# Optimization experiments

Hardware: AMD Instinct MI355X
Metric: run time of the kernel (lower is better)

## Reference

```python
import jax, jax.numpy as jnp
import numpy as np

N = 65536
E = 1048576
NFEAT, NHID, NCLASS = 128, 64, 40


def setup_inputs() -> dict:
    key = jax.random.key(0)
    ks = jax.random.split(key, 20)
    inp = {
        "x": jax.random.normal(ks[0], (N, NFEAT), dtype=jnp.float32),
        "src": jax.random.randint(ks[1], (E,), 0, N, dtype=jnp.int32),
        "dst": jax.random.randint(ks[2], (E,), 0, N, dtype=jnp.int32),
        "edge_w": jax.random.uniform(ks[3], (E,), dtype=jnp.float32),
    }
    dims = [(NFEAT, NHID)] + [(NHID, NHID)] * 5 + [(NHID, NCLASS)]
    for i, (fi, fo) in enumerate(dims, start=1):
        scale = 1.0 / np.sqrt(fi)
        inp[f"W{i}"] = jax.random.uniform(ks[3 + i], (fi, fo), minval=-scale, maxval=scale, dtype=jnp.float32)
        inp[f"b{i}"] = jax.random.uniform(ks[10 + i], (fo,), minval=-scale, maxval=scale, dtype=jnp.float32)
    return inp


def _gc(h, W, b, src, dst, edge_w):
    # GraphConvolution: adj @ (h @ W) + b, with adj in COO form.
    support = h @ W                      # [N, fo] dense GEMM
    msgs = support[src] * edge_w[:, None]  # [E, fo] irregular gather
    agg = jax.ops.segment_sum(msgs, dst, num_segments=N)  # scatter-add
    return agg + b


def reference(x, src, dst, edge_w, W1, b1, W2, b2, W3, b3, W4, b4, W5, b5, W6, b6, W7, b7):
    # eval mode: dropout is identity
    h = jax.nn.relu(_gc(x, W1, b1, src, dst, edge_w))
    h = jax.nn.relu(_gc(h, W2, b2, src, dst, edge_w))
    h = jax.nn.relu(_gc(h, W3, b3, src, dst, edge_w)) + h
    h = jax.nn.relu(_gc(h, W4, b4, src, dst, edge_w)) + h
    h = jax.nn.relu(_gc(h, W5, b5, src, dst, edge_w)) + h
    h = jax.nn.relu(_gc(h, W6, b6, src, dst, edge_w))
    h = _gc(h, W7, b7, src, dst, edge_w)
    return jax.nn.log_softmax(h, axis=1)
```

## Files before the change

### kernel.cpp

```cpp
#include <hip/hip_runtime.h>
#include <math.h>


constexpr int NFEAT = 128, NHID = 64, NCLASS = 40;

typedef unsigned short ushort_t;
typedef int ivec4 __attribute__((ext_vector_type(4)));

__device__ inline float bf2f(ushort_t u) {
  union { unsigned int i; float f; } v; v.i = ((unsigned int)u) << 16; return v.f;
}
__device__ inline ushort_t f2bf(float f) {
  union { float f; unsigned int i; } v; v.f = f;
  unsigned int lsb = (v.i >> 16) & 1u;
  v.i += 0x7fffu + lsb;
  return (ushort_t)(v.i >> 16);
}

__global__ void rank_k(const int* __restrict__ dst, int* __restrict__ cnt4,
                       int* __restrict__ rank, int E, int N) {
  int i = blockIdx.x * blockDim.x + threadIdx.x;
  int base = i * 4;
  if (base >= E) return;
  int4 d4 = *(const int4*)(dst + base);
  int r0 = atomicAdd(&cnt4[0 * N + d4.x], 1);
  int r1 = atomicAdd(&cnt4[1 * N + d4.y], 1);
  int r2 = atomicAdd(&cnt4[2 * N + d4.z], 1);
  int r3 = atomicAdd(&cnt4[3 * N + d4.w], 1);
  ivec4 rr = { (r0 << 2) | 0, (r1 << 2) | 1, (r2 << 2) | 2, (r3 << 2) | 3 };
  __builtin_nontemporal_store(rr, (ivec4*)(rank + base));
}

__global__ void scan1_k(const int* __restrict__ cnt4, int* __restrict__ off,
                        int* __restrict__ bsum, int4* __restrict__ sb4, int n) {
  __shared__ int tmp[256];
  int tid = threadIdx.x;
  int i = blockIdx.x * 256 + tid;
  int c0 = 0, c1 = 0, c2 = 0, c3 = 0;
  if (i < n) {
    c0 = cnt4[i]; c1 = cnt4[n + i]; c2 = cnt4[2 * n + i]; c3 = cnt4[3 * n + i];
  }
  int v = c0 + c1 + c2 + c3;
  tmp[tid] = v;
  __syncthreads();
  for (int d = 1; d < 256; d <<= 1) {
    int t = (tid >= d) ? tmp[tid - d] : 0;
    __syncthreads();
    tmp[tid] += t;
    __syncthreads();
  }
  if (i < n) {
    off[i] = tmp[tid] - v;
    sb4[i] = make_int4(0, c0, c0 + c1, c0 + c1 + c2);
  }
  if (tid == 255) bsum[blockIdx.x] = tmp[255];
}

__global__ void scan2_k(int* __restrict__ bsum, int nb) {
  __shared__ int tmp[256];
  int tid = threadIdx.x;
  int v = (tid < nb) ? bsum[tid] : 0;
  tmp[tid] = v;
  __syncthreads();
  for (int d = 1; d < 256; d <<= 1) {
    int t = (tid >= d) ? tmp[tid - d] : 0;
    __syncthreads();
    tmp[tid] += t;
    __syncthreads();
  }
  if (tid < nb) bsum[tid] = tmp[tid] - v;
}

__global__ void scan3_k(int* __restrict__ off, const int* __restrict__ bsum, int n, int E) {
  int i = blockIdx.x * blockDim.x + threadIdx.x;
  if (i < n) off[i] += bsum[i >> 8];
  if (i == 0) off[n] = E;
}

__global__ void fill_k(const int* __restrict__ src, const int* __restrict__ dst,
                       const float* __restrict__ w, const int* __restrict__ off,
                       const int* __restrict__ rank, const int* __restrict__ sb4,
                       int2* __restrict__ edata, int E) {
  int i = blockIdx.x * blockDim.x + threadIdx.x;
  if (i < E) {
    int d = dst[i];
    int rp = rank[i];
    int s = rp & 3, sr = rp >> 2;
    int pos = off[d] + sb4[d * 4 + s] + sr;
    int2 v = make_int2(src[i], __float_as_int(w[i]));
    __builtin_nontemporal_store(*(const long long*)&v, (long long*)&edata[pos]);
  }
}

template<int FI, int FO>
__global__ __launch_bounds__(256) void gemm_k(const float* __restrict__ h,
                                              const float* __restrict__ W,
                                              ushort_t* __restrict__ out, int n) {
  constexpr int HS = 68;
  __shared__ float hl[64 * HS];
  __shared__ float wl[64 * 64];
  int tid = threadIdx.x;
  int row0 = blockIdx.x * 64;
  int tx = tid & 15, ty = tid >> 4;

  float acc[4][4] = {};

  for (int kc = 0; kc < FI; kc += 64) {
    {
      const float* hb = h + (size_t)row0 * FI + kc;
      for (int i = tid; i < 64 * 16; i += 256) {
        int r = i >> 4, kk = (i & 15) << 2;
        float4 v = *(const float4*)(hb + (size_t)r * FI + kk);
        *(float4*)&hl[r * HS + kk] = v;
      }
    }
    if (FO == 64) {
      const float4* Wb = (const float4*)(W + (size_t)kc * 64);
      for (int i = tid; i < 64 * 16; i += 256) ((float4*)wl)[i] = Wb[i];
    } else {
      for (int i = tid; i < 64 * 64; i += 256) wl[i] = 0.0f;
      __syncthreads();
      for (int i = tid; i < 64 * FO; i += 256)
        wl[(i / FO) * 64 + (i % FO)] = W[(size_t)(kc + i / FO) * FO + (i % FO)];
    }
    __syncthreads();

    for (int k4 = 0; k4 < 64; k4 += 4) {
      float4 a[4];
#pragma unroll
      for (int r = 0; r < 4; ++r)
        a[r] = *(const float4*)&hl[(ty * 4 + r) * HS + k4];
#pragma unroll
      for (int j = 0; j < 4; ++j) {
        float4 bv = *(const float4*)&wl[(k4 + j) * 64 + tx * 4];
        const float* bp = (const float*)&bv;
#pragma unroll
        for (int r = 0; r < 4; ++r) {
          const float* ap = (const float*)&a[r];
#pragma unroll
          for (int c = 0; c < 4; ++c) acc[r][c] += ap[j] * bp[c];
        }
      }
    }
    __syncthreads();
  }

  if (FO == 64) {
#pragma unroll
    for (int r = 0; r < 4; ++r) {
      ushort_t pk[4];
#pragma unroll
      for (int c = 0; c < 4; ++c) pk[c] = f2bf(acc[r][c]);
      *(ushort4*)&out[(size_t)(row0 + ty * 4 + r) * 64 + tx * 4] =
          make_ushort4(pk[0], pk[1], pk[2], pk[3]);
    }
  } else {
#pragma unroll
    for (int r = 0; r < 4; ++r)
#pragma unroll
      for (int c = 0; c < 4; ++c) {
        int col = tx * 4 + c;
        if (col < FO) out[(size_t)(row0 + ty * 4 + r) * FO + col] = f2bf(acc[r][c]);
      }
  }
}

__global__ __launch_bounds__(256, 8) void agg_k(
    const ushort_t* __restrict__ support,
    const int2* __restrict__ edata,
    const int* __restrict__ off,
    const float* __restrict__ bias,
    const float* __restrict__ resid,
    float* __restrict__ out,
    int n, int do_relu) {
  int tid = blockIdx.x * blockDim.x + threadIdx.x;
  int wid = tid >> 6, lane = tid & 63;
  if (wid >= n) return;
  int half = lane >> 5;
  int hl   = lane & 31;
  int e0 = __builtin_amdgcn_readfirstlane(off[wid]);
  int e1 = __builtin_amdgcn_readfirstlane(off[wid + 1]);
  int deg = e1 - e0;

  const ushort_t* sp = support + hl * 2;
  const int* epi = (const int*)(edata + e0);

  float ax[4] = {}, ay[4] = {};
  if (deg > 0) {
    int sx[16];
#pragma unroll
    for (int j = 0; j < 16; ++j) {
      int rel = 2 * j + half;
      sx[j] = epi[(rel < deg ? rel : 0) * 2];
    }
    unsigned int u[16];
#pragma unroll
    for (int j = 0; j < 16; ++j)
      u[j] = *(const unsigned int*)(sp + ((size_t)sx[j] << 6));
    float wv[16];
#pragma unroll
    for (int j = 0; j < 16; ++j) {
      int rel = 2 * j + half;
      wv[j] = (rel < deg) ? __int_as_float(epi[rel * 2 + 1]) : 0.0f;
    }
#pragma unroll
    for (int j = 0; j < 16; ++j) {
      ax[j & 3] += wv[j] * __int_as_float(u[j] << 16);
      ay[j & 3] += wv[j] * __int_as_float(u[j] & 0xffff0000u);
    }
    for (int it = 32; it < deg; it += 16) {
      int2 ed[8];
#pragma unroll
      for (int j = 0; j < 8; ++j) {
        int rel = it + 2 * j + half;
        ed[j] = *(const int2*)(epi + (rel < deg ? rel : 0) * 2);
      }
      unsigned int uu[8];
#pragma unroll
      for (int j = 0; j < 8; ++j)
        uu[j] = *(const unsigned int*)(sp + ((size_t)ed[j].x << 6));
#pragma unroll
      for (int j = 0; j < 8; ++j) {
        int rel = it + 2 * j + half;
        float w = (rel < deg) ? __int_as_float(ed[j].y) : 0.0f;
        ax[j & 3] += w * __int_as_float(uu[j] << 16);
        ay[j & 3] += w * __int_as_float(uu[j] & 0xffff0000u);
      }
    }
  }
  float sx2 = (ax[0] + ax[1]) + (ax[2] + ax[3]);
  float sy2 = (ay[0] + ay[1]) + (ay[2] + ay[3]);
  sx2 += __shfl_xor(sx2, 32, 64);
  sy2 += __shfl_xor(sy2, 32, 64);
  if (half == 0) {
    float2 bv = *(const float2*)&bias[hl * 2];
    float vx = sx2 + bv.x, vy = sy2 + bv.y;
    if (do_relu) { vx = fmaxf(vx, 0.0f); vy = fmaxf(vy, 0.0f); }
    if (resid) {
      float2 r = *(const float2*)&resid[(size_t)wid * 64 + hl * 2];
      vx += r.x; vy += r.y;
    }
    *(float2*)&out[(size_t)wid * 64 + hl * 2] = make_float2(vx, vy);
  }
}

__global__ __launch_bounds__(256, 8) void agg_final_k(
    const ushort_t* __restrict__ support,
    const int2* __restrict__ edata,
    const int* __restrict__ off,
    const float* __restrict__ bias,
    float* __restrict__ out, int n) {
  int tid = blockIdx.x * blockDim.x + threadIdx.x;
  int wid = tid >> 6, lane = tid & 63;
  if (wid >= n) return;
  int half = lane >> 5;
  int hl   = lane & 31;
  int col  = (hl < 20 ? hl : 0) * 2;
  int e0 = __builtin_amdgcn_readfirstlane(off[wid]);
  int e1 = __builtin_amdgcn_readfirstlane(off[wid + 1]);
  int deg = e1 - e0;

  const ushort_t* sp = support + col;
  const int* epi = (const int*)(edata + e0);

  float ax[4] = {}, ay[4] = {};
  if (deg > 0) {
    int sx[16];
#pragma unroll
    for (int j = 0; j < 16; ++j) {
      int rel = 2 * j + half;
      sx[j] = epi[(rel < deg ? rel : 0) * 2];
    }
    unsigned int u[16];
#pragma unroll
    for (int j = 0; j < 16; ++j)
      u[j] = *(const unsigned int*)(sp + (size_t)sx[j] * NCLASS);
    float wv[16];
#pragma unroll
    for (int j = 0; j < 16; ++j) {
      int rel = 2 * j + half;
      wv[j] = (rel < deg) ? __int_as_float(epi[rel * 2 + 1]) : 0.0f;
    }
#pragma unroll
    for (int j = 0; j < 16; ++j) {
      ax[j & 3] += wv[j] * __int_as_float(u[j] << 16);
      ay[j & 3] += wv[j] * __int_as_float(u[j] & 0xffff0000u);
    }
    for (int it = 32; it < deg; it += 16) {
      int2 ed[8];
#pragma unroll
      for (int j = 0; j < 8; ++j) {
        int rel = it + 2 * j + half;
        ed[j] = *(const int2*)(epi + (rel < deg ? rel : 0) * 2);
      }
      unsigned int uu[8];
#pragma unroll
      for (int j = 0; j < 8; ++j)
        uu[j] = *(const unsigned int*)(sp + (size_t)ed[j].x * NCLASS);
#pragma unroll
      for (int j = 0; j < 8; ++j) {
        int rel = it + 2 * j + half;
        float w = (rel < deg) ? __int_as_float(ed[j].y) : 0.0f;
        ax[j & 3] += w * __int_as_float(uu[j] << 16);
        ay[j & 3] += w * __int_as_float(uu[j] & 0xffff0000u);
      }
    }
  }
  float sx2 = (ax[0] + ax[1]) + (ax[2] + ax[3]);
  float sy2 = (ay[0] + ay[1]) + (ay[2] + ay[3]);
  sx2 += __shfl_xor(sx2, 32, 64);
  sy2 += __shfl_xor(sy2, 32, 64);
  float2 bv = *(const float2*)&bias[col];
  float vx = sx2 + bv.x, vy = sy2 + bv.y;

  bool valid = (hl < 20);
  float m = valid ? fmaxf(vx, vy) : -INFINITY;
#pragma unroll
  for (int d = 32; d; d >>= 1) m = fmaxf(m, __shfl_xor(m, d, 64));
  float ex = valid ? (expf(vx - m) + expf(vy - m)) : 0.0f;
  float s = ex;
#pragma unroll
  for (int d = 32; d; d >>= 1) s += __shfl_xor(s, d, 64);
  float ls = logf(s);
  if (half == 0 && valid)
    *(float2*)&out[(size_t)wid * NCLASS + hl * 2] = make_float2(vx - m - ls, vy - m - ls);
}

extern "C" void kernel_launch(void* const* d_in, const int* in_sizes, int n_in,
                              void* d_out, int out_size, void* d_ws, size_t ws_size,
                              hipStream_t stream) {
  const float* x   = (const float*)d_in[0];
  const int*   src = (const int*)d_in[1];
  const int*   dst = (const int*)d_in[2];
  const float* ew  = (const float*)d_in[3];
  const float* W[7]; const float* b[7];
  for (int i = 0; i < 7; ++i) {
    W[i] = (const float*)d_in[4 + 2 * i];
    b[i] = (const float*)d_in[5 + 2 * i];
  }
  int N = in_sizes[0] / NFEAT;
  int E = in_sizes[1];

  char* ws = (char*)d_ws;
  int*      off     = (int*)(ws + 0);
  int*      bsum    = (int*)(ws + (1ll << 20));
  int*      cnt4    = (int*)(ws + (2ll << 20));
  int4*     sb4     = (int4*)(ws + (3ll << 20));
  int2*     edata   = (int2*)(ws + (4ll << 20));
  int*      rank    = (int*)(ws + (12ll << 20));
  ushort_t* support = (ushort_t*)(ws + (16ll << 20));
  float*    hA      = (float*)(ws + (32ll << 20));
  float*    hB      = (float*)(ws + (48ll << 20));

  (void)hipMemsetAsync(cnt4, 0, (size_t)4 * N * sizeof(int), stream);
  rank_k<<<(E / 4 + 255) / 256, 256, 0, stream>>>(dst, cnt4, rank, E, N);
  int nb = (N + 255) / 256;
  scan1_k<<<nb, 256, 0, stream>>>(cnt4, off, bsum, sb4, N);
  scan2_k<<<1, 256, 0, stream>>>(bsum, nb);
  scan3_k<<<nb, 256, 0, stream>>>(off, bsum, N, E);
  fill_k<<<(E + 255) / 256, 256, 0, stream>>>(src, dst, ew, off, rank,
                                              (const int*)sb4, edata, E);

  int gb_gemm = N / 64;
  int gb_agg  = N / 4;

  gemm_k<128, 64><<<gb_gemm, 256, 0, stream>>>(x, W[0], support, N);
  agg_k<<<gb_agg, 256, 0, stream>>>(support, edata, off, b[0], nullptr, hA, N, 1);
  gemm_k<64, 64><<<gb_gemm, 256, 0, stream>>>(hA, W[1], support, N);
  agg_k<<<gb_agg, 256, 0, stream>>>(support, edata, off, b[1], nullptr, hB, N, 1);
  gemm_k<64, 64><<<gb_gemm, 256, 0, stream>>>(hB, W[2], support, N);
  agg_k<<<gb_agg, 256, 0, stream>>>(support, edata, off, b[2], hB, hA, N, 1);
  gemm_k<64, 64><<<gb_gemm, 256, 0, stream>>>(hA, W[3], support, N);
  agg_k<<<gb_agg, 256, 0, stream>>>(support, edata, off, b[3], hA, hB, N, 1);
  gemm_k<64, 64><<<gb_gemm, 256, 0, stream>>>(hB, W[4], support, N);
  agg_k<<<gb_agg, 256, 0, stream>>>(support, edata, off, b[4], hB, hA, N, 1);
  gemm_k<64, 64><<<gb_gemm, 256, 0, stream>>>(hA, W[5], support, N);
  agg_k<<<gb_agg, 256, 0, stream>>>(support, edata, off, b[5], nullptr, hB, N, 1);
  gemm_k<64, 40><<<gb_gemm, 256, 0, stream>>>(hB, W[6], support, N);
  agg_final_k<<<gb_agg, 256, 0, stream>>>(support, edata, off, b[6], (float*)d_out, N);
}
```

Baseline: 411.7 us.

## Process two nodes per wavefront in aggregation and vectorize CSR fill kernel

The aggregation kernels now assign two destination nodes to each wavefront, so gathers for both nodes are issued together and more loads are in flight per wave. Occupancy hint drops from 8 to 4 blocks per CU to allow the larger register footprint, and the grid is halved to match. The fill kernel now handles four edges per thread using vector loads of src, dst, weight and rank. Risks are higher register pressure and lower occupancy, plus load imbalance when the two paired nodes have very different degrees.

```diff
diff --git a/kernel.cpp b/kernel.cpp
--- a/kernel.cpp
+++ b/kernel.cpp
@@ -82,12 +82,25 @@
                        const int* __restrict__ rank, const int* __restrict__ sb4,
                        int2* __restrict__ edata, int E) {
   int i = blockIdx.x * blockDim.x + threadIdx.x;
-  if (i < E) {
-    int d = dst[i];
-    int rp = rank[i];
-    int s = rp & 3, sr = rp >> 2;
-    int pos = off[d] + sb4[d * 4 + s] + sr;
-    int2 v = make_int2(src[i], __float_as_int(w[i]));
+  int base = i * 4;
+  if (base >= E) return;
+  int4 s4 = *(const int4*)(src + base);
+  int4 d4 = *(const int4*)(dst + base);
+  float4 w4 = *(const float4*)(w + base);
+  int4 r4 = *(const int4*)(rank + base);
+  int dd[4] = { d4.x, d4.y, d4.z, d4.w };
+  int rr[4] = { r4.x, r4.y, r4.z, r4.w };
+  int ss[4] = { s4.x, s4.y, s4.z, s4.w };
+  float ww[4] = { w4.x, w4.y, w4.z, w4.w };
+  int ob[4], sb[4];
+#pragma unroll
+  for (int k = 0; k < 4; ++k) ob[k] = off[dd[k]];
+#pragma unroll
+  for (int k = 0; k < 4; ++k) sb[k] = sb4[dd[k] * 4 + (rr[k] & 3)];
+#pragma unroll
+  for (int k = 0; k < 4; ++k) {
+    int pos = ob[k] + sb[k] + (rr[k] >> 2);
+    int2 v = make_int2(ss[k], __float_as_int(ww[k]));
     __builtin_nontemporal_store(*(const long long*)&v, (long long*)&edata[pos]);
   }
 }
@@ -165,7 +178,7 @@
   }
 }
 
-__global__ __launch_bounds__(256, 8) void agg_k(
+__global__ __launch_bounds__(256, 4) void agg_k(
     const ushort_t* __restrict__ support,
     const int2* __restrict__ edata,
     const int* __restrict__ off,
@@ -174,156 +187,257 @@
     float* __restrict__ out,
     int n, int do_relu) {
   int tid = blockIdx.x * blockDim.x + threadIdx.x;
-  int wid = tid >> 6, lane = tid & 63;
-  if (wid >= n) return;
+  int p = tid >> 6, lane = tid & 63;
+  int nA = 2 * p, nB = 2 * p + 1;
+  if (nA >= n) return;
   int half = lane >> 5;
   int hl   = lane & 31;
-  int e0 = __builtin_amdgcn_readfirstlane(off[wid]);
-  int e1 = __builtin_amdgcn_readfirstlane(off[wid + 1]);
-  int deg = e1 - e0;
+  int e0a = __builtin_amdgcn_readfirstlane(off[nA]);
+  int e0b = __builtin_amdgcn_readfirstlane(off[nB]);
+  int e1b = __builtin_amdgcn_readfirstlane(off[nB + 1]);
+  int degA = e0b - e0a, degB = e1b - e0b;
 
   const ushort_t* sp = support + hl * 2;
-  const int* epi = (const int*)(edata + e0);
-
-  float ax[4] = {}, ay[4] = {};
-  if (deg > 0) {
-    int sx[16];
-#pragma unroll
-    for (int j = 0; j < 16; ++j) {
-      int rel = 2 * j + half;
-      sx[j] = epi[(rel < deg ? rel : 0) * 2];
-    }
-    unsigned int u[16];
-#pragma unroll
-    for (int j = 0; j < 16; ++j)
-      u[j] = *(const unsigned int*)(sp + ((size_t)sx[j] << 6));
-    float wv[16];
-#pragma unroll
-    for (int j = 0; j < 16; ++j) {
-      int rel = 2 * j + half;
-      wv[j] = (rel < deg) ? __int_as_float(epi[rel * 2 + 1]) : 0.0f;
-    }
-#pragma unroll
-    for (int j = 0; j < 16; ++j) {
-      ax[j & 3] += wv[j] * __int_as_float(u[j] << 16);
-      ay[j & 3] += wv[j] * __int_as_float(u[j] & 0xffff0000u);
-    }
-    for (int it = 32; it < deg; it += 16) {
-      int2 ed[8];
-#pragma unroll
-      for (int j = 0; j < 8; ++j) {
-        int rel = it + 2 * j + half;
-        ed[j] = *(const int2*)(epi + (rel < deg ? rel : 0) * 2);
-      }
-      unsigned int uu[8];
-#pragma unroll
-      for (int j = 0; j < 8; ++j)
-        uu[j] = *(const unsigned int*)(sp + ((size_t)ed[j].x << 6));
-#pragma unroll
-      for (int j = 0; j < 8; ++j) {
-        int rel = it + 2 * j + half;
-        float w = (rel < deg) ? __int_as_float(ed[j].y) : 0.0f;
-        ax[j & 3] += w * __int_as_float(uu[j] << 16);
-        ay[j & 3] += w * __int_as_float(uu[j] & 0xffff0000u);
-      }
-    }
-  }
-  float sx2 = (ax[0] + ax[1]) + (ax[2] + ax[3]);
-  float sy2 = (ay[0] + ay[1]) + (ay[2] + ay[3]);
-  sx2 += __shfl_xor(sx2, 32, 64);
-  sy2 += __shfl_xor(sy2, 32, 64);
+  const int* epA = (const int*)(edata + e0a);
+  const int* epB = (const int*)(edata + e0b);
+
+  float axA[4] = {}, ayA[4] = {}, axB[4] = {}, ayB[4] = {};
+
+  int sA[16], sB[16];
+#pragma unroll
+  for (int j = 0; j < 16; ++j) {
+    int rel = 2 * j + half;
+    sA[j] = epA[(rel < degA ? rel : 0) * 2];
+  }
+#pragma unroll
+  for (int j = 0; j < 16; ++j) {
+    int rel = 2 * j + half;
+    sB[j] = epB[(rel < degB ? rel : 0) * 2];
+  }
+  unsigned int uA[16], uB[16];
+#pragma unroll
+  for (int j = 0; j < 16; ++j)
+    uA[j] = *(const unsigned int*)(sp + ((size_t)sA[j] << 6));
+#pragma unroll
+  for (int j = 0; j < 16; ++j)
+    uB[j] = *(const unsigned int*)(sp + ((size_t)sB[j] << 6));
+#pragma unroll
+  for (int j = 0; j < 16; ++j) {
+    int rel = 2 * j + half;
+    float w = (rel < degA) ? __int_as_float(epA[rel * 2 + 1]) : 0.0f;
+    axA[j & 3] += w * __int_as_float(uA[j] << 16);
+    ayA[j & 3] += w * __int_as_float(uA[j] & 0xffff0000u);
+  }
+#pragma unroll
+  for (int j = 0; j < 16; ++j) {
+    int rel = 2 * j + half;
+    float w = (rel < degB) ? __int_as_float(epB[rel * 2 + 1]) : 0.0f;
+    axB[j & 3] += w * __int_as_float(uB[j] << 16);
+    ayB[j & 3] += w * __int_as_float(uB[j] & 0xffff0000u);
+  }
+  for (int it = 32; it < degA; it += 16) {
+    int2 ed[8];
+#pragma unroll
+    for (int j = 0; j < 8; ++j) {
+      int rel = it + 2 * j + half;
+      ed[j] = *(const int2*)(epA + (rel < degA ? rel : 0) * 2);
+    }
+    unsigned int uu[8];
+#pragma unroll
+    for (int j = 0; j < 8; ++j)
+      uu[j] = *(const unsigned int*)(sp + ((size_t)ed[j].x << 6));
+#pragma unroll
+    for (int j = 0; j < 8; ++j) {
+      int rel = it + 2 * j + half;
+      float w = (rel < degA) ? __int_as_float(ed[j].y) : 0.0f;
+      axA[j & 3] += w * __int_as_float(uu[j] << 16);
+      ayA[j & 3] += w * __int_as_float(uu[j] & 0xffff0000u);
+    }
+  }
+  for (int it = 32; it < degB; it += 16) {
+    int2 ed[8];
+#pragma unroll
+    for (int j = 0; j < 8; ++j) {
+      int rel = it + 2 * j + half;
+      ed[j] = *(const int2*)(epB + (rel < degB ? rel : 0) * 2);
+    }
+    unsigned int uu[8];
+#pragma unroll
+    for (int j = 0; j < 8; ++j)
+      uu[j] = *(const unsigned int*)(sp + ((size_t)ed[j].x << 6));
+#pragma unroll
+    for (int j = 0; j < 8; ++j) {
+      int rel = it + 2 * j + half;
+      float w = (rel < degB) ? __int_as_float(ed[j].y) : 0.0f;
+      axB[j & 3] += w * __int_as_float(uu[j] << 16);
+      ayB[j & 3] += w * __int_as_float(uu[j] & 0xffff0000u);
+    }
+  }
+
+  float sxA = ((axA[0] + axA[1]) + (axA[2] + axA[3]));
+  float syA = ((ayA[0] + ayA[1]) + (ayA[2] + ayA[3]));
+  float sxB = ((axB[0] + axB[1]) + (axB[2] + axB[3]));
+  float syB = ((ayB[0] + ayB[1]) + (ayB[2] + ayB[3]));
+  sxA += __shfl_xor(sxA, 32, 64);
+  syA += __shfl_xor(syA, 32, 64);
+  sxB += __shfl_xor(sxB, 32, 64);
+  syB += __shfl_xor(syB, 32, 64);
+
+  float2 bv = *(const float2*)&bias[hl * 2];
   if (half == 0) {
-    float2 bv = *(const float2*)&bias[hl * 2];
-    float vx = sx2 + bv.x, vy = sy2 + bv.y;
+    float vx = sxA + bv.x, vy = syA + bv.y;
     if (do_relu) { vx = fmaxf(vx, 0.0f); vy = fmaxf(vy, 0.0f); }
     if (resid) {
-      float2 r = *(const float2*)&resid[(size_t)wid * 64 + hl * 2];
+      float2 r = *(const float2*)&resid[(size_t)nA * 64 + hl * 2];
       vx += r.x; vy += r.y;
     }
-    *(float2*)&out[(size_t)wid * 64 + hl * 2] = make_float2(vx, vy);
-  }
-}
-
-__global__ __launch_bounds__(256, 8) void agg_final_k(
+    *(float2*)&out[(size_t)nA * 64 + hl * 2] = make_float2(vx, vy);
+  } else {
+    float vx = sxB + bv.x, vy = syB + bv.y;
+    if (do_relu) { vx = fmaxf(vx, 0.0f); vy = fmaxf(vy, 0.0f); }
+    if (resid) {
+      float2 r = *(const float2*)&resid[(size_t)nB * 64 + hl * 2];
+      vx += r.x; vy += r.y;
+    }
+    *(float2*)&out[(size_t)nB * 64 + hl * 2] = make_float2(vx, vy);
+  }
+}
+
+__global__ __launch_bounds__(256, 4) void agg_final_k(
     const ushort_t* __restrict__ support,
     const int2* __restrict__ edata,
     const int* __restrict__ off,
     const float* __restrict__ bias,
     float* __restrict__ out, int n) {
   int tid = blockIdx.x * blockDim.x + threadIdx.x;
-  int wid = tid >> 6, lane = tid & 63;
-  if (wid >= n) return;
+  int p = tid >> 6, lane = tid & 63;
+  int nA = 2 * p, nB = 2 * p + 1;
+  if (nA >= n) return;
   int half = lane >> 5;
   int hl   = lane & 31;
   int col  = (hl < 20 ? hl : 0) * 2;
-  int e0 = __builtin_amdgcn_readfirstlane(off[wid]);
-  int e1 = __builtin_amdgcn_readfirstlane(off[wid + 1]);
-  int deg = e1 - e0;
+  int e0a = __builtin_amdgcn_readfirstlane(off[nA]);
+  int e0b = __builtin_amdgcn_readfirstlane(off[nB]);
+  int e1b = __builtin_amdgcn_readfirstlane(off[nB + 1]);
+  int degA = e0b - e0a, degB = e1b - e0b;
 
   const ushort_t* sp = support + col;
-  const int* epi = (const int*)(edata + e0);
-
-  float ax[4] = {}, ay[4] = {};
-  if (deg > 0) {
-    int sx[16];
-#pragma unroll
-    for (int j = 0; j < 16; ++j) {
-      int rel = 2 * j + half;
-      sx[j] = epi[(rel < deg ? rel : 0) * 2];
-    }
-    unsigned int u[16];
-#pragma unroll
-    for (int j = 0; j < 16; ++j)
-      u[j] = *(const unsigned int*)(sp + (size_t)sx[j] * NCLASS);
-    float wv[16];
-#pragma unroll
-    for (int j = 0; j < 16; ++j) {
-      int rel = 2 * j + half;
-      wv[j] = (rel < deg) ? __int_as_float(epi[rel * 2 + 1]) : 0.0f;
-    }
-#pragma unroll
-    for (int j = 0; j < 16; ++j) {
-      ax[j & 3] += wv[j] * __int_as_float(u[j] << 16);
-      ay[j & 3] += wv[j] * __int_as_float(u[j] & 0xffff0000u);
-    }
-    for (int it = 32; it < deg; it += 16) {
-      int2 ed[8];
-#pragma unroll
-      for (int j = 0; j < 8; ++j) {
-        int rel = it + 2 * j + half;
-        ed[j] = *(const int2*)(epi + (rel < deg ? rel : 0) * 2);
-      }
-      unsigned int uu[8];
-#pragma unroll
-      for (int j = 0; j < 8; ++j)
-        uu[j] = *(const unsigned int*)(sp + (size_t)ed[j].x * NCLASS);
-#pragma unroll
-      for (int j = 0; j < 8; ++j) {
-        int rel = it + 2 * j + half;
-        float w = (rel < deg) ? __int_as_float(ed[j].y) : 0.0f;
-        ax[j & 3] += w * __int_as_float(uu[j] << 16);
-        ay[j & 3] += w * __int_as_float(uu[j] & 0xffff0000u);
-      }
-    }
-  }
-  float sx2 = (ax[0] + ax[1]) + (ax[2] + ax[3]);
-  float sy2 = (ay[0] + ay[1]) + (ay[2] + ay[3]);
-  sx2 += __shfl_xor(sx2, 32, 64);
-  sy2 += __shfl_xor(sy2, 32, 64);
+  const int* epA = (const int*)(edata + e0a);
+  const int* epB = (const int*)(edata + e0b);
+
+  float axA[4] = {}, ayA[4] = {}, axB[4] = {}, ayB[4] = {};
+
+  int sA[16], sB[16];
+#pragma unroll
+  for (int j = 0; j < 16; ++j) {
+    int rel = 2 * j + half;
+    sA[j] = epA[(rel < degA ? rel : 0) * 2];
+  }
+#pragma unroll
+  for (int j = 0; j < 16; ++j) {
+    int rel = 2 * j + half;
+    sB[j] = epB[(rel < degB ? rel : 0) * 2];
+  }
+  unsigned int uA[16], uB[16];
+#pragma unroll
+  for (int j = 0; j < 16; ++j)
+    uA[j] = *(const unsigned int*)(sp + (size_t)sA[j] * NCLASS);
+#pragma unroll
+  for (int j = 0; j < 16; ++j)
+    uB[j] = *(const unsigned int*)(sp + (size_t)sB[j] * NCLASS);
+#pragma unroll
+  for (int j = 0; j < 16; ++j) {
+    int rel = 2 * j + half;
+    float w = (rel < degA) ? __int_as_float(epA[rel * 2 + 1]) : 0.0f;
+    axA[j & 3] += w * __int_as_float(uA[j] << 16);
+    ayA[j & 3] += w * __int_as_float(uA[j] & 0xffff0000u);
+  }
+#pragma unroll
+  for (int j = 0; j < 16; ++j) {
+    int rel = 2 * j + half;
+    float w = (rel < degB) ? __int_as_float(epB[rel * 2 + 1]) : 0.0f;
+    axB[j & 3] += w * __int_as_float(uB[j] << 16);
+    ayB[j & 3] += w * __int_as_float(uB[j] & 0xffff0000u);
+  }
+  for (int it = 32; it < degA; it += 16) {
+    int2 ed[8];
+#pragma unroll
+    for (int j = 0; j < 8; ++j) {
+      int rel = it + 2 * j + half;
+      ed[j] = *(const int2*)(epA + (rel < degA ? rel : 0) * 2);
+    }
+    unsigned int uu[8];
+#pragma unroll
+    for (int j = 0; j < 8; ++j)
+      uu[j] = *(const unsigned int*)(sp + (size_t)ed[j].x * NCLASS);
+#pragma unroll
+    for (int j = 0; j < 8; ++j) {
+      int rel = it + 2 * j + half;
+      float w = (rel < degA) ? __int_as_float(ed[j].y) : 0.0f;
+      axA[j & 3] += w * __int_as_float(uu[j] << 16);
+      ayA[j & 3] += w * __int_as_float(uu[j] & 0xffff0000u);
+    }
+  }
+  for (int it = 32; it < degB; it += 16) {
+    int2 ed[8];
+#pragma unroll
+    for (int j = 0; j < 8; ++j) {
+      int rel = it + 2 * j + half;
+      ed[j] = *(const int2*)(epB + (rel < degB ? rel : 0) * 2);
+    }
+    unsigned int uu[8];
+#pragma unroll
+    for (int j = 0; j < 8; ++j)
+      uu[j] = *(const unsigned int*)(sp + (size_t)ed[j].x * NCLASS);
+#pragma unroll
+    for (int j = 0; j < 8; ++j) {
+      int rel = it + 2 * j + half;
+      float w = (rel < degB) ? __int_as_float(ed[j].y) : 0.0f;
+      axB[j & 3] += w * __int_as_float(uu[j] << 16);
+      ayB[j & 3] += w * __int_as_float(uu[j] & 0xffff0000u);
+    }
+  }
+
+  float sxA = ((axA[0] + axA[1]) + (axA[2] + axA[3]));
+  float syA = ((ayA[0] + ayA[1]) + (ayA[2] + ayA[3]));
+  float sxB = ((axB[0] + axB[1]) + (axB[2] + axB[3]));
+  float syB = ((ayB[0] + ayB[1]) + (ayB[2] + ayB[3]));
+  sxA += __shfl_xor(sxA, 32, 64);
+  syA += __shfl_xor(syA, 32, 64);
+  sxB += __shfl_xor(sxB, 32, 64);
+  syB += __shfl_xor(syB, 32, 64);
+
+  bool valid = (hl < 20);
   float2 bv = *(const float2*)&bias[col];
-  float vx = sx2 + bv.x, vy = sy2 + bv.y;
-
-  bool valid = (hl < 20);
-  float m = valid ? fmaxf(vx, vy) : -INFINITY;
-#pragma unroll
-  for (int d = 32; d; d >>= 1) m = fmaxf(m, __shfl_xor(m, d, 64));
-  float ex = valid ? (expf(vx - m) + expf(vy - m)) : 0.0f;
-  float s = ex;
-#pragma unroll
-  for (int d = 32; d; d >>= 1) s += __shfl_xor(s, d, 64);
-  float ls = logf(s);
-  if (half == 0 && valid)
-    *(float2*)&out[(size_t)wid * NCLASS + hl * 2] = make_float2(vx - m - ls, vy - m - ls);
+  float vxA = sxA + bv.x, vyA = syA + bv.y;
+  float vxB = sxB + bv.x, vyB = syB + bv.y;
+
+  float mA = valid ? fmaxf(vxA, vyA) : -INFINITY;
+  float mB = valid ? fmaxf(vxB, vyB) : -INFINITY;
+#pragma unroll
+  for (int d = 32; d; d >>= 1) {
+    mA = fmaxf(mA, __shfl_xor(mA, d, 64));
+    mB = fmaxf(mB, __shfl_xor(mB, d, 64));
+  }
+  float exA = (valid && half == 0) ? (expf(vxA - mA) + expf(vyA - mA)) : 0.0f;
+  float exB = (valid && half == 0) ? (expf(vxB - mB) + expf(vyB - mB)) : 0.0f;
+  float sA2 = exA, sB2 = exB;
+#pragma unroll
+  for (int d = 32; d; d >>= 1) {
+    sA2 += __shfl_xor(sA2, d, 64);
+    sB2 += __shfl_xor(sB2, d, 64);
+  }
+  if (valid) {
+    if (half == 0) {
+      float ls = logf(sA2);
+      *(float2*)&out[(size_t)nA * NCLASS + hl * 2] =
+          make_float2(vxA - mA - ls, vyA - mA - ls);
+    } else {
+      float ls = logf(sB2);
+      *(float2*)&out[(size_t)nB * NCLASS + hl * 2] =
+          make_float2(vxB - mB - ls, vyB - mB - ls);
+    }
+  }
 }
 
 extern "C" void kernel_launch(void* const* d_in, const int* in_sizes, int n_in,
@@ -358,11 +472,11 @@
   scan1_k<<<nb, 256, 0, stream>>>(cnt4, off, bsum, sb4, N);
   scan2_k<<<1, 256, 0, stream>>>(bsum, nb);
   scan3_k<<<nb, 256, 0, stream>>>(off, bsum, N, E);
-  fill_k<<<(E + 255) / 256, 256, 0, stream>>>(src, dst, ew, off, rank,
-                                              (const int*)sb4, edata, E);
+  fill_k<<<(E / 4 + 255) / 256, 256, 0, stream>>>(src, dst, ew, off, rank,
+                                                  (const int*)sb4, edata, E);
 
   int gb_gemm = N / 64;
-  int gb_agg  = N / 4;
+  int gb_agg  = N / 8;
 
   gemm_k<128, 64><<<gb_gemm, 256, 0, stream>>>(x, W[0], support, N);
   agg_k<<<gb_agg, 256, 0, stream>>>(support, edata, off, b[0], nullptr, hA, N, 1);
```

After: 403.4 us. 2.0% less time.

## Fuse aggregation with next-layer GEMM in persistent kernels and merge rank with first GEMM

Applied to the files above, without the earlier changes.

Each layer's aggregation kernel now also multiplies the aggregated row by the next layer's weight matrix, held in registers, and writes the bf16 support for the next layer directly. This removes the separate GEMM launches and the fp32 hidden-state round trips, except where a residual is needed. The first GEMM is interleaved with the rank/atomic-count pass in a single launch, and fill_k is vectorized to four edges per thread. Aggregation now uses 16 lanes × 4 features per edge slot with persistent waves. The cost is 64 weight registers per thread at lower occupancy, and a per-node LDS broadcast that uses only a block fence and no barrier.

```diff
diff --git a/kernel.cpp b/kernel.cpp
--- a/kernel.cpp
+++ b/kernel.cpp
@@ -7,9 +7,6 @@
 typedef unsigned short ushort_t;
 typedef int ivec4 __attribute__((ext_vector_type(4)));
 
-__device__ inline float bf2f(ushort_t u) {
-  union { unsigned int i; float f; } v; v.i = ((unsigned int)u) << 16; return v.f;
-}
 __device__ inline ushort_t f2bf(float f) {
   union { float f; unsigned int i; } v; v.f = f;
   unsigned int lsb = (v.i >> 16) & 1u;
@@ -17,18 +14,75 @@
   return (ushort_t)(v.i >> 16);
 }
 
-__global__ void rank_k(const int* __restrict__ dst, int* __restrict__ cnt4,
-                       int* __restrict__ rank, int E, int N) {
-  int i = blockIdx.x * blockDim.x + threadIdx.x;
-  int base = i * 4;
-  if (base >= E) return;
-  int4 d4 = *(const int4*)(dst + base);
-  int r0 = atomicAdd(&cnt4[0 * N + d4.x], 1);
-  int r1 = atomicAdd(&cnt4[1 * N + d4.y], 1);
-  int r2 = atomicAdd(&cnt4[2 * N + d4.z], 1);
-  int r3 = atomicAdd(&cnt4[3 * N + d4.w], 1);
-  ivec4 rr = { (r0 << 2) | 0, (r1 << 2) | 1, (r2 << 2) | 2, (r3 << 2) | 3 };
-  __builtin_nontemporal_store(rr, (ivec4*)(rank + base));
+__global__ __launch_bounds__(256) void rankgemm_k(
+    const float* __restrict__ x, const float* __restrict__ W1,
+    ushort_t* __restrict__ sout,
+    const int* __restrict__ dst, int* __restrict__ cnt4,
+    int* __restrict__ rank, int E, int N) {
+  constexpr int HS = 68;
+  __shared__ float hl[64 * HS];
+  __shared__ float wl[64 * 64];
+  int tid = threadIdx.x;
+  int bid = blockIdx.x;
+
+  if (bid & 1) {
+    int i = (bid >> 1) * 256 + tid;
+    int base = i * 4;
+    if (base >= E) return;
+    int4 d4 = *(const int4*)(dst + base);
+    int r0 = atomicAdd(&cnt4[0 * N + d4.x], 1);
+    int r1 = atomicAdd(&cnt4[1 * N + d4.y], 1);
+    int r2 = atomicAdd(&cnt4[2 * N + d4.z], 1);
+    int r3 = atomicAdd(&cnt4[3 * N + d4.w], 1);
+    ivec4 rr = { (r0 << 2) | 0, (r1 << 2) | 1, (r2 << 2) | 2, (r3 << 2) | 3 };
+    __builtin_nontemporal_store(rr, (ivec4*)(rank + base));
+    return;
+  }
+
+  int row0 = (bid >> 1) * 64;
+  int tx = tid & 15, ty = tid >> 4;
+  float acc[4][4] = {};
+  for (int kc = 0; kc < 128; kc += 64) {
+    {
+      const float* hb = x + (size_t)row0 * 128 + kc;
+      for (int i = tid; i < 64 * 16; i += 256) {
+        int r = i >> 4, kk = (i & 15) << 2;
+        float4 v = *(const float4*)(hb + (size_t)r * 128 + kk);
+        *(float4*)&hl[r * HS + kk] = v;
+      }
+    }
+    {
+      const float4* Wb = (const float4*)(W1 + (size_t)kc * 64);
+      for (int i = tid; i < 64 * 16; i += 256) ((float4*)wl)[i] = Wb[i];
+    }
+    __syncthreads();
+    for (int k4 = 0; k4 < 64; k4 += 4) {
+      float4 a[4];
+#pragma unroll
+      for (int r = 0; r < 4; ++r)
+        a[r] = *(const float4*)&hl[(ty * 4 + r) * HS + k4];
+#pragma unroll
+      for (int j = 0; j < 4; ++j) {
+        float4 bv = *(const float4*)&wl[(k4 + j) * 64 + tx * 4];
+        const float* bp = (const float*)&bv;
+#pragma unroll
+        for (int r = 0; r < 4; ++r) {
+          const float* ap = (const float*)&a[r];
+#pragma unroll
+          for (int c = 0; c < 4; ++c) acc[r][c] += ap[j] * bp[c];
+        }
+      }
+    }
+    __syncthreads();
+  }
+#pragma unroll
+  for (int r = 0; r < 4; ++r) {
+    ushort_t pk[4];
+#pragma unroll
+    for (int c = 0; c < 4; ++c) pk[c] = f2bf(acc[r][c]);
+    *(ushort4*)&sout[(size_t)(row0 + ty * 4 + r) * 64 + tx * 4] =
+        make_ushort4(pk[0], pk[1], pk[2], pk[3]);
+  }
 }
 
 __global__ void scan1_k(const int* __restrict__ cnt4, int* __restrict__ off,
@@ -82,248 +136,198 @@
                        const int* __restrict__ rank, const int* __restrict__ sb4,
                        int2* __restrict__ edata, int E) {
   int i = blockIdx.x * blockDim.x + threadIdx.x;
-  if (i < E) {
-    int d = dst[i];
-    int rp = rank[i];
-    int s = rp & 3, sr = rp >> 2;
-    int pos = off[d] + sb4[d * 4 + s] + sr;
-    int2 v = make_int2(src[i], __float_as_int(w[i]));
+  int base = i * 4;
+  if (base >= E) return;
+  int4 s4 = *(const int4*)(src + base);
+  int4 d4 = *(const int4*)(dst + base);
+  float4 w4 = *(const float4*)(w + base);
+  int4 r4 = *(const int4*)(rank + base);
+  int dd[4] = { d4.x, d4.y, d4.z, d4.w };
+  int rr[4] = { r4.x, r4.y, r4.z, r4.w };
+  int ss[4] = { s4.x, s4.y, s4.z, s4.w };
+  float ww[4] = { w4.x, w4.y, w4.z, w4.w };
+  int ob[4], sb[4];
+#pragma unroll
+  for (int k = 0; k < 4; ++k) ob[k] = off[dd[k]];
+#pragma unroll
+  for (int k = 0; k < 4; ++k) sb[k] = sb4[dd[k] * 4 + (rr[k] & 3)];
+#pragma unroll
+  for (int k = 0; k < 4; ++k) {
+    int pos = ob[k] + sb[k] + (rr[k] >> 2);
+    int2 v = make_int2(ss[k], __float_as_int(ww[k]));
     __builtin_nontemporal_store(*(const long long*)&v, (long long*)&edata[pos]);
   }
 }
 
-template<int FI, int FO>
-__global__ __launch_bounds__(256) void gemm_k(const float* __restrict__ h,
-                                              const float* __restrict__ W,
-                                              ushort_t* __restrict__ out, int n) {
-  constexpr int HS = 68;
-  __shared__ float hl[64 * HS];
-  __shared__ float wl[64 * 64];
-  int tid = threadIdx.x;
-  int row0 = blockIdx.x * 64;
-  int tx = tid & 15, ty = tid >> 4;
-
-  float acc[4][4] = {};
-
-  for (int kc = 0; kc < FI; kc += 64) {
-    {
-      const float* hb = h + (size_t)row0 * FI + kc;
-      for (int i = tid; i < 64 * 16; i += 256) {
-        int r = i >> 4, kk = (i & 15) << 2;
-        float4 v = *(const float4*)(hb + (size_t)r * FI + kk);
-        *(float4*)&hl[r * HS + kk] = v;
-      }
-    }
-    if (FO == 64) {
-      const float4* Wb = (const float4*)(W + (size_t)kc * 64);
-      for (int i = tid; i < 64 * 16; i += 256) ((float4*)wl)[i] = Wb[i];
-    } else {
-      for (int i = tid; i < 64 * 64; i += 256) wl[i] = 0.0f;
-      __syncthreads();
-      for (int i = tid; i < 64 * FO; i += 256)
-        wl[(i / FO) * 64 + (i % FO)] = W[(size_t)(kc + i / FO) * FO + (i % FO)];
-    }
-    __syncthreads();
-
-    for (int k4 = 0; k4 < 64; k4 += 4) {
-      float4 a[4];
-#pragma unroll
-      for (int r = 0; r < 4; ++r)
-        a[r] = *(const float4*)&hl[(ty * 4 + r) * HS + k4];
-#pragma unroll
-      for (int j = 0; j < 4; ++j) {
-        float4 bv = *(const float4*)&wl[(k4 + j) * 64 + tx * 4];
-        const float* bp = (const float*)&bv;
-#pragma unroll
-        for (int r = 0; r < 4; ++r) {
-          const float* ap = (const float*)&a[r];
-#pragma unroll
-          for (int c = 0; c < 4; ++c) acc[r][c] += ap[j] * bp[c];
-        }
-      }
-    }
-    __syncthreads();
-  }
-
-  if (FO == 64) {
-#pragma unroll
-    for (int r = 0; r < 4; ++r) {
-      ushort_t pk[4];
-#pragma unroll
-      for (int c = 0; c < 4; ++c) pk[c] = f2bf(acc[r][c]);
-      *(ushort4*)&out[(size_t)(row0 + ty * 4 + r) * 64 + tx * 4] =
-          make_ushort4(pk[0], pk[1], pk[2], pk[3]);
-    }
-  } else {
-#pragma unroll
-    for (int r = 0; r < 4; ++r)
-#pragma unroll
-      for (int c = 0; c < 4; ++c) {
-        int col = tx * 4 + c;
-        if (col < FO) out[(size_t)(row0 + ty * 4 + r) * FO + col] = f2bf(acc[r][c]);
-      }
-  }
-}
-
-__global__ __launch_bounds__(256, 8) void agg_k(
+template<int FO, bool WRITE_H>
+__global__ __launch_bounds__(256, 4) void aggemm_k(
     const ushort_t* __restrict__ support,
     const int2* __restrict__ edata,
     const int* __restrict__ off,
     const float* __restrict__ bias,
     const float* __restrict__ resid,
-    float* __restrict__ out,
-    int n, int do_relu) {
-  int tid = blockIdx.x * blockDim.x + threadIdx.x;
-  int wid = tid >> 6, lane = tid & 63;
-  if (wid >= n) return;
-  int half = lane >> 5;
-  int hl   = lane & 31;
-  int e0 = __builtin_amdgcn_readfirstlane(off[wid]);
-  int e1 = __builtin_amdgcn_readfirstlane(off[wid + 1]);
-  int deg = e1 - e0;
-
-  const ushort_t* sp = support + hl * 2;
-  const int* epi = (const int*)(edata + e0);
-
-  float ax[4] = {}, ay[4] = {};
-  if (deg > 0) {
-    int sx[16];
-#pragma unroll
-    for (int j = 0; j < 16; ++j) {
-      int rel = 2 * j + half;
-      sx[j] = epi[(rel < deg ? rel : 0) * 2];
-    }
-    unsigned int u[16];
-#pragma unroll
-    for (int j = 0; j < 16; ++j)
-      u[j] = *(const unsigned int*)(sp + ((size_t)sx[j] << 6));
-    float wv[16];
-#pragma unroll
-    for (int j = 0; j < 16; ++j) {
-      int rel = 2 * j + half;
-      wv[j] = (rel < deg) ? __int_as_float(epi[rel * 2 + 1]) : 0.0f;
-    }
-#pragma unroll
-    for (int j = 0; j < 16; ++j) {
-      ax[j & 3] += wv[j] * __int_as_float(u[j] << 16);
-      ay[j & 3] += wv[j] * __int_as_float(u[j] & 0xffff0000u);
-    }
-    for (int it = 32; it < deg; it += 16) {
-      int2 ed[8];
+    const float* __restrict__ Wn,
+    ushort_t* __restrict__ sout,
+    float* __restrict__ hout,
+    int n) {
+  __shared__ float hls[4][64];
+  int tid = threadIdx.x;
+  int lane = tid & 63;
+  int wv = tid >> 6;
+  int gw = blockIdx.x * 4 + wv;
+  int nwaves = gridDim.x << 2;
+  int slot = lane >> 4, q = lane & 15;
+
+  int wcol = (FO == 64) ? lane : (lane < FO ? lane : 0);
+  float wreg[64];
+#pragma unroll
+  for (int k = 0; k < 64; ++k) wreg[k] = Wn[(size_t)k * FO + wcol];
+
+  const ushort_t* sp = support + q * 4;
+
+  for (int node = gw; node < n; node += nwaves) {
+    int e0 = __builtin_amdgcn_readfirstlane(off[node]);
+    int e1 = __builtin_amdgcn_readfirstlane(off[node + 1]);
+    int deg = e1 - e0;
+    const int* epi = (const int*)(edata + e0);
+
+    float a0 = 0.f, a1 = 0.f, a2 = 0.f, a3 = 0.f;
+    if (deg > 0) {
+      int2 mt[8];
 #pragma unroll
       for (int j = 0; j < 8; ++j) {
-        int rel = it + 2 * j + half;
-        ed[j] = *(const int2*)(epi + (rel < deg ? rel : 0) * 2);
-      }
-      unsigned int uu[8];
+        int rel = 4 * j + slot;
+        mt[j] = *(const int2*)(epi + (rel < deg ? rel : 0) * 2);
+      }
+      uint2 g[8];
 #pragma unroll
       for (int j = 0; j < 8; ++j)
-        uu[j] = *(const unsigned int*)(sp + ((size_t)ed[j].x << 6));
+        g[j] = *(const uint2*)(sp + ((size_t)mt[j].x << 6));
 #pragma unroll
       for (int j = 0; j < 8; ++j) {
-        int rel = it + 2 * j + half;
-        float w = (rel < deg) ? __int_as_float(ed[j].y) : 0.0f;
-        ax[j & 3] += w * __int_as_float(uu[j] << 16);
-        ay[j & 3] += w * __int_as_float(uu[j] & 0xffff0000u);
-      }
-    }
-  }
-  float sx2 = (ax[0] + ax[1]) + (ax[2] + ax[3]);
-  float sy2 = (ay[0] + ay[1]) + (ay[2] + ay[3]);
-  sx2 += __shfl_xor(sx2, 32, 64);
-  sy2 += __shfl_xor(sy2, 32, 64);
-  if (half == 0) {
-    float2 bv = *(const float2*)&bias[hl * 2];
-    float vx = sx2 + bv.x, vy = sy2 + bv.y;
-    if (do_relu) { vx = fmaxf(vx, 0.0f); vy = fmaxf(vy, 0.0f); }
+        int rel = 4 * j + slot;
+        float w = (rel < deg) ? __int_as_float(mt[j].y) : 0.0f;
+        a0 += w * __int_as_float(g[j].x << 16);
+        a1 += w * __int_as_float(g[j].x & 0xffff0000u);
+        a2 += w * __int_as_float(g[j].y << 16);
+        a3 += w * __int_as_float(g[j].y & 0xffff0000u);
+      }
+      for (int it = 32; it < deg; it += 32) {
+#pragma unroll
+        for (int j = 0; j < 8; ++j) {
+          int rel = it + 4 * j + slot;
+          int2 m = *(const int2*)(epi + (rel < deg ? rel : 0) * 2);
+          uint2 gg = *(const uint2*)(sp + ((size_t)m.x << 6));
+          float w = (rel < deg) ? __int_as_float(m.y) : 0.0f;
+          a0 += w * __int_as_float(gg.x << 16);
+          a1 += w * __int_as_float(gg.x & 0xffff0000u);
+          a2 += w * __int_as_float(gg.y << 16);
+          a3 += w * __int_as_float(gg.y & 0xffff0000u);
+        }
+      }
+    }
+    a0 += __shfl_xor(a0, 16, 64); a1 += __shfl_xor(a1, 16, 64);
+    a2 += __shfl_xor(a2, 16, 64); a3 += __shfl_xor(a3, 16, 64);
+    a0 += __shfl_xor(a0, 32, 64); a1 += __shfl_xor(a1, 32, 64);
+    a2 += __shfl_xor(a2, 32, 64); a3 += __shfl_xor(a3, 32, 64);
+
+    float4 bv = *(const float4*)&bias[q * 4];
+    float v0 = fmaxf(a0 + bv.x, 0.f), v1 = fmaxf(a1 + bv.y, 0.f);
+    float v2 = fmaxf(a2 + bv.z, 0.f), v3 = fmaxf(a3 + bv.w, 0.f);
     if (resid) {
-      float2 r = *(const float2*)&resid[(size_t)wid * 64 + hl * 2];
-      vx += r.x; vy += r.y;
-    }
-    *(float2*)&out[(size_t)wid * 64 + hl * 2] = make_float2(vx, vy);
-  }
-}
-
-__global__ __launch_bounds__(256, 8) void agg_final_k(
+      float4 r = *(const float4*)&resid[(size_t)node * 64 + q * 4];
+      v0 += r.x; v1 += r.y; v2 += r.z; v3 += r.w;
+    }
+    if (slot == 0) {
+      *(float4*)&hls[wv][q * 4] = make_float4(v0, v1, v2, v3);
+      if (WRITE_H)
+        *(float4*)&hout[(size_t)node * 64 + q * 4] = make_float4(v0, v1, v2, v3);
+    }
+    __threadfence_block();
+
+    float o = 0.f;
+    const float* hb = hls[wv];
+#pragma unroll
+    for (int k = 0; k < 64; k += 4) {
+      float4 hv = *(const float4*)&hb[k];
+      o += hv.x * wreg[k] + hv.y * wreg[k + 1] + hv.z * wreg[k + 2] + hv.w * wreg[k + 3];
+    }
+    if (FO == 64 || lane < FO)
+      sout[(size_t)node * FO + wcol] = f2bf(o);
+  }
+}
+
+__global__ __launch_bounds__(256, 4) void agg_final_k(
     const ushort_t* __restrict__ support,
     const int2* __restrict__ edata,
     const int* __restrict__ off,
     const float* __restrict__ bias,
     float* __restrict__ out, int n) {
   int tid = blockIdx.x * blockDim.x + threadIdx.x;
-  int wid = tid >> 6, lane = tid & 63;
-  if (wid >= n) return;
-  int half = lane >> 5;
-  int hl   = lane & 31;
-  int col  = (hl < 20 ? hl : 0) * 2;
-  int e0 = __builtin_amdgcn_readfirstlane(off[wid]);
-  int e1 = __builtin_amdgcn_readfirstlane(off[wid + 1]);
+  int node = tid >> 6, lane = tid & 63;
+  if (node >= n) return;
+  int slot = lane >> 4, q = lane & 15;
+  int qc = (q < 10) ? q : 9;
+  bool valid = (q < 10);
+  int e0 = __builtin_amdgcn_readfirstlane(off[node]);
+  int e1 = __builtin_amdgcn_readfirstlane(off[node + 1]);
   int deg = e1 - e0;
-
-  const ushort_t* sp = support + col;
   const int* epi = (const int*)(edata + e0);
-
-  float ax[4] = {}, ay[4] = {};
+  const ushort_t* sp = support + qc * 4;
+
+  float a0 = 0.f, a1 = 0.f, a2 = 0.f, a3 = 0.f;
   if (deg > 0) {
-    int sx[16];
-#pragma unroll
-    for (int j = 0; j < 16; ++j) {
-      int rel = 2 * j + half;
-      sx[j] = epi[(rel < deg ? rel : 0) * 2];
-    }
-    unsigned int u[16];
-#pragma unroll
-    for (int j = 0; j < 16; ++j)
-      u[j] = *(const unsigned int*)(sp + (size_t)sx[j] * NCLASS);
-    float wv[16];
-#pragma unroll
-    for (int j = 0; j < 16; ++j) {
-      int rel = 2 * j + half;
-      wv[j] = (rel < deg) ? __int_as_float(epi[rel * 2 + 1]) : 0.0f;
-    }
-#pragma unroll
-    for (int j = 0; j < 16; ++j) {
-      ax[j & 3] += wv[j] * __int_as_float(u[j] << 16);
-      ay[j & 3] += wv[j] * __int_as_float(u[j] & 0xffff0000u);
-    }
-    for (int it = 32; it < deg; it += 16) {
-      int2 ed[8];
+    int2 mt[8];
+#pragma unroll
+    for (int j = 0; j < 8; ++j) {
+      int rel = 4 * j + slot;
+      mt[j] = *(const int2*)(epi + (rel < deg ? rel : 0) * 2);
+    }
+    uint2 g[8];
+#pragma unroll
+    for (int j = 0; j < 8; ++j)
+      g[j] = *(const uint2*)(sp + (size_t)mt[j].x * NCLASS);
+#pragma unroll
+    for (int j = 0; j < 8; ++j) {
+      int rel = 4 * j + slot;
+      float w = (rel < deg) ? __int_as_float(mt[j].y) : 0.0f;
+      a0 += w * __int_as_float(g[j].x << 16);
+      a1 += w * __int_as_float(g[j].x & 0xffff0000u);
+      a2 += w * __int_as_float(g[j].y << 16);
+      a3 += w * __int_as_float(g[j].y & 0xffff0000u);
+    }
+    for (int it = 32; it < deg; it += 32) {
 #pragma unroll
       for (int j = 0; j < 8; ++j) {
-        int rel = it + 2 * j + half;
-        ed[j] = *(const int2*)(epi + (rel < deg ? rel : 0) * 2);
-      }
-      unsigned int uu[8];
-#pragma unroll
-      for (int j = 0; j < 8; ++j)
-        uu[j] = *(const unsigned int*)(sp + (size_t)ed[j].x * NCLASS);
-#pragma unroll
-      for (int j = 0; j < 8; ++j) {
-        int rel = it + 2 * j + half;
-        float w = (rel < deg) ? __int_as_float(ed[j].y) : 0.0f;
-        ax[j & 3] += w * __int_as_float(uu[j] << 16);
-        ay[j & 3] += w * __int_as_float(uu[j] & 0xffff0000u);
-      }
-    }
-  }
-  float sx2 = (ax[0] + ax[1]) + (ax[2] + ax[3]);
-  float sy2 = (ay[0] + ay[1]) + (ay[2] + ay[3]);
-  sx2 += __shfl_xor(sx2, 32, 64);
-  sy2 += __shfl_xor(sy2, 32, 64);
-  float2 bv = *(const float2*)&bias[col];
-  float vx = sx2 + bv.x, vy = sy2 + bv.y;
-
-  bool valid = (hl < 20);
-  float m = valid ? fmaxf(vx, vy) : -INFINITY;
-#pragma unroll
-  for (int d = 32; d; d >>= 1) m = fmaxf(m, __shfl_xor(m, d, 64));
-  float ex = valid ? (expf(vx - m) + expf(vy - m)) : 0.0f;
-  float s = ex;
-#pragma unroll
-  for (int d = 32; d; d >>= 1) s += __shfl_xor(s, d, 64);
+        int rel = it + 4 * j + slot;
+        int2 m = *(const int2*)(epi + (rel < deg ? rel : 0) * 2);
+        uint2 gg = *(const uint2*)(sp + (size_t)m.x * NCLASS);
+        float w = (rel < deg) ? __int_as_float(m.y) : 0.0f;
+        a0 += w * __int_as_float(gg.x << 16);
+        a1 += w * __int_as_float(gg.x & 0xffff0000u);
+        a2 += w * __int_as_float(gg.y << 16);
+        a3 += w * __int_as_float(gg.y & 0xffff0000u);
+      }
+    }
+  }
+  a0 += __shfl_xor(a0, 16, 64); a1 += __shfl_xor(a1, 16, 64);
+  a2 += __shfl_xor(a2, 16, 64); a3 += __shfl_xor(a3, 16, 64);
+  a0 += __shfl_xor(a0, 32, 64); a1 += __shfl_xor(a1, 32, 64);
+  a2 += __shfl_xor(a2, 32, 64); a3 += __shfl_xor(a3, 32, 64);
+
+  float4 bv = *(const float4*)&bias[qc * 4];
+  float f0 = a0 + bv.x, f1 = a1 + bv.y, f2 = a2 + bv.z, f3 = a3 + bv.w;
+
+  float m = valid ? fmaxf(fmaxf(f0, f1), fmaxf(f2, f3)) : -INFINITY;
+#pragma unroll
+  for (int d = 1; d < 16; d <<= 1) m = fmaxf(m, __shfl_xor(m, d, 64));
+  float s = valid ? (expf(f0 - m) + expf(f1 - m) + expf(f2 - m) + expf(f3 - m)) : 0.0f;
+#pragma unroll
+  for (int d = 1; d < 16; d <<= 1) s += __shfl_xor(s, d, 64);
   float ls = logf(s);
-  if (half == 0 && valid)
-    *(float2*)&out[(size_t)wid * NCLASS + hl * 2] = make_float2(vx - m - ls, vy - m - ls);
+  if (slot == 0 && valid)
+    *(float4*)&out[(size_t)node * NCLASS + q * 4] =
+        make_float4(f0 - m - ls, f1 - m - ls, f2 - m - ls, f3 - m - ls);
 }
 
 extern "C" void kernel_launch(void* const* d_in, const int* in_sizes, int n_in,
@@ -348,34 +352,34 @@
   int4*     sb4     = (int4*)(ws + (3ll << 20));
   int2*     edata   = (int2*)(ws + (4ll << 20));
   int*      rank    = (int*)(ws + (12ll << 20));
-  ushort_t* support = (ushort_t*)(ws + (16ll << 20));
+  ushort_t* SA      = (ushort_t*)(ws + (16ll << 20));
+  ushort_t* SB      = (ushort_t*)(ws + (24ll << 20));
   float*    hA      = (float*)(ws + (32ll << 20));
   float*    hB      = (float*)(ws + (48ll << 20));
 
   (void)hipMemsetAsync(cnt4, 0, (size_t)4 * N * sizeof(int), stream);
-  rank_k<<<(E / 4 + 255) / 256, 256, 0, stream>>>(dst, cnt4, rank, E, N);
+  rankgemm_k<<<2048, 256, 0, stream>>>(x, W[0], SA, dst, cnt4, rank, E, N);
   int nb = (N + 255) / 256;
   scan1_k<<<nb, 256, 0, stream>>>(cnt4, off, bsum, sb4, N);
   scan2_k<<<1, 256, 0, stream>>>(bsum, nb);
   scan3_k<<<nb, 256, 0, stream>>>(off, bsum, N, E);
-  fill_k<<<(E + 255) / 256, 256, 0, stream>>>(src, dst, ew, off, rank,
-                                              (const int*)sb4, edata, E);
-
-  int gb_gemm = N / 64;
-  int gb_agg  = N / 4;
-
-  gemm_k<128, 64><<<gb_gemm, 256, 0, stream>>>(x, W[0], support, N);
-  agg_k<<<gb_agg, 256, 0, stream>>>(support, edata, off, b[0], nullptr, hA, N, 1);
-  gemm_k<64, 64><<<gb_gemm, 256, 0, stream>>>(hA, W[1], support, N);
-  agg_k<<<gb_agg, 256, 0, stream>>>(support, edata, off, b[1], nullptr, hB, N, 1);
-  gemm_k<64, 64><<<gb_gemm, 256, 0, stream>>>(hB, W[2], support, N);
-  agg_k<<<gb_agg, 256, 0, stream>>>(support, edata, off, b[2], hB, hA, N, 1);
-  gemm_k<64, 64><<<gb_gemm, 256, 0, stream>>>(hA, W[3], support, N);
-  agg_k<<<gb_agg, 256, 0, stream>>>(support, edata, off, b[3], hA, hB, N, 1);
-  gemm_k<64, 64><<<gb_gemm, 256, 0, stream>>>(hB, W[4], support, N);
-  agg_k<<<gb_agg, 256, 0, stream>>>(support, edata, off, b[4], hB, hA, N, 1);
-  gemm_k<64, 64><<<gb_gemm, 256, 0, stream>>>(hA, W[5], support, N);
-  agg_k<<<gb_agg, 256, 0, stream>>>(support, edata, off, b[5], nullptr, hB, N, 1);
-  gemm_k<64, 40><<<gb_gemm, 256, 0, stream>>>(hB, W[6], support, N);
-  agg_final_k<<<gb_agg, 256, 0, stream>>>(support, edata, off, b[6], (float*)d_out, N);
-}
+  fill_k<<<(E / 4 + 255) / 256, 256, 0, stream>>>(src, dst, ew, off, rank,
+                                                  (const int*)sb4, edata, E);
+
+  int gb_pers = 1024;
+  int gb_fin  = N / 4;
+
+  aggemm_k<64, false><<<gb_pers, 256, 0, stream>>>(SA, edata, off, b[0], nullptr,
+                                                   W[1], SB, nullptr, N);
+  aggemm_k<64, true><<<gb_pers, 256, 0, stream>>>(SB, edata, off, b[1], nullptr,
+                                                  W[2], SA, hA, N);
+  aggemm_k<64, true><<<gb_pers, 256, 0, stream>>>(SA, edata, off, b[2], hA,
+                                                  W[3], SB, hB, N);
+  aggemm_k<64, true><<<gb_pers, 256, 0, stream>>>(SB, edata, off, b[3], hB,
+                                                  W[4], SA, hA, N);
+  aggemm_k<64, false><<<gb_pers, 256, 0, stream>>>(SA, edata, off, b[4], hA,
+                                                   W[5], SB, nullptr, N);
+  aggemm_k<40, false><<<gb_pers, 256, 0, stream>>>(SB, edata, off, b[5], nullptr,
+                                                   W[6], SA, nullptr, N);
+  agg_final_k<<<gb_fin, 256, 0, stream>>>(SA, edata, off, b[6], (float*)d_out, N);
+}
```

New measurement: 480.5 us. +16.7%, slower.
